# Kernel optimization log

Measured on AMD Instinct MI355X. Metric: run time of the kernel, lower is better.

Reference implementation:

```python
import jax, jax.numpy as jnp
import numpy as np

B, S, H, F, E, K = 2, 2048, 1024, 4096, 8, 2

def setup_inputs() -> dict:
    key = jax.random.key(0)
    ks = jax.random.split(key, 8)
    x = jax.random.normal(ks[0], (B, S, H), dtype=jnp.float32)
    # top_k list stacked on leading axis K; probs as from a softmax-topk router
    selected_probs = jax.random.uniform(ks[1], (K, B, S, 1), dtype=jnp.float32)
    selected_experts = jax.random.randint(ks[2], (K, B, S, 1), 0, E).astype(jnp.int32)
    scale = 0.02
    w1 = jax.random.normal(ks[3], (E, H, F), dtype=jnp.float32) * scale
    b1 = jnp.zeros((E, F), dtype=jnp.float32)
    w2 = jax.random.normal(ks[4], (E, F, H), dtype=jnp.float32) * scale
    b2 = jnp.zeros((E, H), dtype=jnp.float32)
    return {"input": x, "selected_probs": selected_probs,
            "selected_experts": selected_experts,
            "w1": w1, "b1": b1, "w2": w2, "b2": b2}

def reference(input, selected_probs, selected_experts, w1, b1, w2, b2):
    # Dense all-experts FFN: every expert processes every token.
    # h: [E, B, S, F]
    h = jax.nn.gelu(jnp.einsum('bsh,ehf->ebsf', input, w1) + b1[:, None, None, :])
    # expert_outputs: [E, B, S, H]
    expert_out = jnp.einsum('ebsf,efh->ebsh', h, w2) + b2[:, None, None, :]
    # combine weight per expert: sum_k probs_k * (sel_k == e)  -> [E, B, S, 1]
    eids = jnp.arange(E, dtype=selected_experts.dtype)
    mask = (selected_experts[:, None] == eids[None, :, None, None, None]).astype(input.dtype)  # [K,E,B,S,1]
    combine_w = (selected_probs[:, None] * mask).sum(axis=0)  # [E,B,S,1]
    return (combine_w * expert_out).sum(axis=0)  # [B,S,H]
```

## Files before the change

### kernel.cpp

```cpp
#include <hip/hip_runtime.h>
#include <hip/hip_bf16.h>
#include <stdint.h>

#define B_ 2
#define S_ 2048
#define H_ 1024
#define F_ 4096
#define E_ 8
#define KTOP_ 2
#define NTOK (B_*S_)
#define NPAIR (KTOP_*NTOK)
#define NPAIR_PAD (NPAIR+128)

static const size_t WS_XG   = 131072;
static const size_t SZ_XG   = (size_t)NPAIR_PAD * H_ * 2;
static const size_t WS_W1T  = WS_XG + SZ_XG;
static const size_t SZ_W1T  = (size_t)E_ * F_ * H_ * 2;
static const size_t WS_W2T  = WS_W1T + SZ_W1T;
static const size_t SZ_W2T  = (size_t)E_ * H_ * F_ * 2;
static const size_t WS_HBUF = WS_W2T + SZ_W2T;
static const size_t SZ_HBUF = (size_t)NPAIR_PAD * F_ * 2;
static const size_t WS_YBUF = WS_HBUF + SZ_HBUF;
static const size_t SZ_YBUF = (size_t)NPAIR * H_ * 4;

typedef __attribute__((ext_vector_type(8))) short bf16x8;
typedef __attribute__((ext_vector_type(4))) float f32x4;

__device__ __forceinline__ unsigned short f2bf(float f) {
  unsigned int u = __float_as_uint(f);
  u += 0x7fffu + ((u >> 16) & 1u);
  return (unsigned short)(u >> 16);
}

__device__ __forceinline__ void load_lds16(const void* g, void* l) {
  __builtin_amdgcn_global_load_lds(
      (const __attribute__((address_space(1))) unsigned int*)g,
      (__attribute__((address_space(3))) unsigned int*)l, 16, 0, 0);
}

__global__ void k_init(int* meta) {
  if (threadIdx.x < 32) meta[threadIdx.x] = 0;
}

__global__ void k_count(const int* __restrict__ sel, int* meta) {
  int i = blockIdx.x * 256 + threadIdx.x;
  if (i < NPAIR) atomicAdd(&meta[sel[i]], 1);
}

__global__ void k_scan(int* meta) {
  if (threadIdx.x == 0) {
    int acc = 0, t = 0;
    for (int e = 0; e < E_; e++) {
      meta[16 + e] = acc;
      int c = meta[e];
      for (int r0 = 0; r0 < c; r0 += 128) meta[32 + (t++)] = (e << 13) | r0;
      acc += c;
    }
    meta[24] = acc;
    meta[25] = t;
  }
}

__global__ void k_fill(const int* __restrict__ sel, const float* __restrict__ probs,
                       int* meta, int* __restrict__ tok, int* __restrict__ slot,
                       float* __restrict__ prob) {
  int i = blockIdx.x * 256 + threadIdx.x;
  if (i < NPAIR) {
    int e = sel[i];
    int pos = meta[16 + e] + atomicAdd(&meta[8 + e], 1);
    tok[pos]  = i & (NTOK - 1);
    slot[pos] = i;
    prob[pos] = probs[i];
  }
}

__global__ void k_gather(const float* __restrict__ x, const int* __restrict__ tok,
                         unsigned short* __restrict__ Xg) {
  int p = blockIdx.x, t = threadIdx.x;
  int token = tok[p];
  float4 v = ((const float4*)(x + (size_t)token * H_))[t];
  ushort4 o;
  o.x = f2bf(v.x); o.y = f2bf(v.y); o.z = f2bf(v.z); o.w = f2bf(v.w);
  ((ushort4*)(Xg + (size_t)p * H_))[t] = o;
}

__global__ void k_transpose(const float* __restrict__ src, unsigned short* __restrict__ dst,
                            int R, int C) {
  __shared__ float tile[32][33];
  int e = blockIdx.z;
  size_t c0 = (size_t)blockIdx.x * 32, r0 = (size_t)blockIdx.y * 32;
  int tx = threadIdx.x & 31, ty = threadIdx.x >> 5;
  const float* s = src + ((size_t)e * R + r0) * C + c0;
#pragma unroll
  for (int i = 0; i < 4; i++) tile[ty + 8 * i][tx] = s[(size_t)(ty + 8 * i) * C + tx];
  __syncthreads();
  unsigned short* d = dst + ((size_t)e * C + c0) * R + r0;
#pragma unroll
  for (int i = 0; i < 4; i++) d[(size_t)(ty + 8 * i) * R + tx] = f2bf(tile[tx][ty + 8 * i]);
}

template <int K, int EP>
__global__ __launch_bounds__(256, 2) void k_gemm(
    const short* __restrict__ Aall, const short* __restrict__ Wt,
    const float* __restrict__ bias, const int* __restrict__ meta,
    unsigned short* __restrict__ Hbuf, float* __restrict__ ybuf,
    const int* __restrict__ slot, const float* __restrict__ prob) {
  int tile = blockIdx.y;
  if (tile >= meta[25]) return;
  int d  = meta[32 + tile];
  int e  = d >> 13, r0 = d & 8191;
  int ne = meta[e];
  int p0 = meta[16 + e] + r0;
  int n0 = blockIdx.x * 128;
  const int NFULL = (EP == 0) ? F_ : H_;
  const short* A0 = Aall + (size_t)p0 * K;
  const short* B0 = Wt + ((size_t)e * NFULL + n0) * K;

  __shared__ short As[128 * 64];
  __shared__ short Bs[128 * 64];
  int t = threadIdx.x, lane = t & 63, wid = t >> 6;
  int wr = wid >> 1, wc = wid & 1, g = lane >> 4, l15 = lane & 15;
  f32x4 acc[4][4] = {};

  for (int k0 = 0; k0 < K; k0 += 64) {
#pragma unroll
    for (int c = 0; c < 4; c++) {
      int off = c * 4096 + wid * 1024 + lane * 16;
      int row = off >> 7, inb = off & 127;
      int sinb = inb ^ ((row & 7) << 4);
      load_lds16((const char*)A0 + ((size_t)row * K + k0) * 2 + sinb, (char*)As + off);
      load_lds16((const char*)B0 + ((size_t)row * K + k0) * 2 + sinb, (char*)Bs + off);
    }
    __syncthreads();
#pragma unroll
    for (int kk = 0; kk < 2; kk++) {
      bf16x8 af[4], bfr[4];
#pragma unroll
      for (int m = 0; m < 4; m++) {
        int row = wr * 64 + m * 16 + l15;
        af[m] = *(const bf16x8*)((const char*)As + row * 128 +
                                 ((kk * 64 + g * 16) ^ ((row & 7) << 4)));
      }
#pragma unroll
      for (int n = 0; n < 4; n++) {
        int row = wc * 64 + n * 16 + l15;
        bfr[n] = *(const bf16x8*)((const char*)Bs + row * 128 +
                                  ((kk * 64 + g * 16) ^ ((row & 7) << 4)));
      }
#pragma unroll
      for (int m = 0; m < 4; m++)
#pragma unroll
        for (int n = 0; n < 4; n++)
          acc[m][n] = __builtin_amdgcn_mfma_f32_16x16x32_bf16(af[m], bfr[n], acc[m][n], 0, 0, 0);
    }
    __syncthreads();
  }

  if (EP == 0) {
#pragma unroll
    for (int n = 0; n < 4; n++) {
      int col = n0 + wc * 64 + n * 16 + l15;
      float bv = bias[e * F_ + col];
#pragma unroll
      for (int m = 0; m < 4; m++) {
        int rbase = wr * 64 + m * 16 + g * 4;
#pragma unroll
        for (int r = 0; r < 4; r++) {
          int row = rbase + r;
          if (r0 + row < ne) {
            float x = acc[m][n][r] + bv;
            float y = 0.7978845608f * x * (1.f + 0.044715f * x * x);
            y = fminf(y, 20.f);
            float u = __expf(2.f * y);
            float th = (u - 1.f) / (u + 1.f);
            Hbuf[(size_t)(p0 + row) * F_ + col] = f2bf(0.5f * x * (1.f + th));
          }
        }
      }
    }
  } else {
#pragma unroll
    for (int n = 0; n < 4; n++) {
      int col = n0 + wc * 64 + n * 16 + l15;
      float bv = bias[e * H_ + col];
#pragma unroll
      for (int m = 0; m < 4; m++) {
        int rbase = wr * 64 + m * 16 + g * 4;
#pragma unroll
        for (int r = 0; r < 4; r++) {
          int row = rbase + r;
          if (r0 + row < ne) {
            int p = p0 + row;
            ybuf[(size_t)slot[p] * H_ + col] = (acc[m][n][r] + bv) * prob[p];
          }
        }
      }
    }
  }
}

__global__ void k_combine(const float* __restrict__ yb, float* __restrict__ out) {
  size_t i = (size_t)blockIdx.x * 256 + threadIdx.x;
  float4 a = ((const float4*)yb)[i];
  float4 b = ((const float4*)(yb + (size_t)NTOK * H_))[i];
  float4 o;
  o.x = a.x + b.x; o.y = a.y + b.y; o.z = a.z + b.z; o.w = a.w + b.w;
  ((float4*)out)[i] = o;
}

extern "C" void kernel_launch(void* const* d_in, const int* in_sizes, int n_in,
                              void* d_out, int out_size, void* d_ws, size_t ws_size,
                              hipStream_t stream) {
  const float* x     = (const float*)d_in[0];
  const float* probs = (const float*)d_in[1];
  const int*   sel   = (const int*)d_in[2];
  const float* w1    = (const float*)d_in[3];
  const float* b1    = (const float*)d_in[4];
  const float* w2    = (const float*)d_in[5];
  const float* b2    = (const float*)d_in[6];
  float* out = (float*)d_out;

  char* W = (char*)d_ws;
  int*   meta = (int*)W;
  int*   tok  = (int*)(W + 4096);
  int*   slot = (int*)(W + 36864);
  float* prob = (float*)(W + 69632);
  unsigned short* Xg  = (unsigned short*)(W + WS_XG);
  short* w1t = (short*)(W + WS_W1T);
  short* w2t = (short*)(W + WS_W2T);
  unsigned short* Hb  = (unsigned short*)(W + WS_HBUF);
  float* yb  = (float*)(W + WS_YBUF);

  k_init<<<1, 256, 0, stream>>>(meta);
  k_count<<<NPAIR / 256, 256, 0, stream>>>(sel, meta);
  k_scan<<<1, 64, 0, stream>>>(meta);
  k_fill<<<NPAIR / 256, 256, 0, stream>>>(sel, probs, meta, tok, slot, prob);
  k_gather<<<NPAIR, 256, 0, stream>>>(x, tok, Xg);
  k_transpose<<<dim3(F_ / 32, H_ / 32, E_), 256, 0, stream>>>(w1, (unsigned short*)w1t, H_, F_);
  k_transpose<<<dim3(H_ / 32, F_ / 32, E_), 256, 0, stream>>>(w2, (unsigned short*)w2t, F_, H_);
  k_gemm<H_, 0><<<dim3(F_ / 128, 72), 256, 0, stream>>>(
      (const short*)Xg, w1t, b1, meta, Hb, yb, slot, prob);
  k_gemm<F_, 1><<<dim3(H_ / 128, 72), 256, 0, stream>>>(
      (const short*)Hb, w2t, b2, meta, Hb, yb, slot, prob);
  k_combine<<<(NTOK * H_ / 4) / 256, 256, 0, stream>>>(yb, out);
}
```

Measured before the change: 432.2 us.

## Rewrite expert GEMMs with 256-row tiles, 4-stage LDS pipeline and wider transpose

Replaces the 128x128 single-buffered GEMM with a 512-thread kernel using 256-row M tiles and a 4-slot LDS ring. Loads are issued three k-steps ahead, with explicit vmcnt waits, barriers and setprio around the MFMA phases, so global loads overlap compute. The GELU epilogue becomes an exp2 plus reciprocal sigmoid form of the tanh approximation. The weight transpose moves to 64x64 tiles with float4 reads and paired bf16 writes. Larger tiles cut the number of M tiles but add padding waste for experts whose counts are not multiples of 256, and the LDS footprint grows.

```diff
diff --git a/kernel.cpp b/kernel.cpp
--- a/kernel.cpp
+++ b/kernel.cpp
@@ -10,7 +10,7 @@
 #define KTOP_ 2
 #define NTOK (B_*S_)
 #define NPAIR (KTOP_*NTOK)
-#define NPAIR_PAD (NPAIR+128)
+#define NPAIR_PAD (NPAIR+256)
 
 static const size_t WS_XG   = 131072;
 static const size_t SZ_XG   = (size_t)NPAIR_PAD * H_ * 2;
@@ -21,7 +21,6 @@
 static const size_t WS_HBUF = WS_W2T + SZ_W2T;
 static const size_t SZ_HBUF = (size_t)NPAIR_PAD * F_ * 2;
 static const size_t WS_YBUF = WS_HBUF + SZ_HBUF;
-static const size_t SZ_YBUF = (size_t)NPAIR * H_ * 4;
 
 typedef __attribute__((ext_vector_type(8))) short bf16x8;
 typedef __attribute__((ext_vector_type(4))) float f32x4;
@@ -36,6 +35,10 @@
   __builtin_amdgcn_global_load_lds(
       (const __attribute__((address_space(1))) unsigned int*)g,
       (__attribute__((address_space(3))) unsigned int*)l, 16, 0, 0);
+}
+
+template <int N> __device__ __forceinline__ void waitcnt_vm() {
+  asm volatile("s_waitcnt vmcnt(%0)" :: "n"(N) : "memory");
 }
 
 __global__ void k_init(int* meta) {
@@ -53,7 +56,7 @@
     for (int e = 0; e < E_; e++) {
       meta[16 + e] = acc;
       int c = meta[e];
-      for (int r0 = 0; r0 < c; r0 += 128) meta[32 + (t++)] = (e << 13) | r0;
+      for (int r0 = 0; r0 < c; r0 += 256) meta[32 + (t++)] = (e << 13) | r0;
       acc += c;
     }
     meta[24] = acc;
@@ -86,112 +89,209 @@
 
 __global__ void k_transpose(const float* __restrict__ src, unsigned short* __restrict__ dst,
                             int R, int C) {
-  __shared__ float tile[32][33];
+  __shared__ float tile[64][65];
   int e = blockIdx.z;
-  size_t c0 = (size_t)blockIdx.x * 32, r0 = (size_t)blockIdx.y * 32;
-  int tx = threadIdx.x & 31, ty = threadIdx.x >> 5;
-  const float* s = src + ((size_t)e * R + r0) * C + c0;
-#pragma unroll
-  for (int i = 0; i < 4; i++) tile[ty + 8 * i][tx] = s[(size_t)(ty + 8 * i) * C + tx];
+  size_t c0 = (size_t)blockIdx.x * 64, r0 = (size_t)blockIdx.y * 64;
+  int t = threadIdx.x;
+  int r = t >> 2, q = t & 3;
+  const float4* s = (const float4*)(src + ((size_t)e * R + r0 + r) * C + c0 + q * 16);
+  float4 v0 = s[0], v1 = s[1], v2 = s[2], v3 = s[3];
+  float* tp = &tile[r][q * 16];
+  tp[0]=v0.x; tp[1]=v0.y; tp[2]=v0.z; tp[3]=v0.w;
+  tp[4]=v1.x; tp[5]=v1.y; tp[6]=v1.z; tp[7]=v1.w;
+  tp[8]=v2.x; tp[9]=v2.y; tp[10]=v2.z; tp[11]=v2.w;
+  tp[12]=v3.x; tp[13]=v3.y; tp[14]=v3.z; tp[15]=v3.w;
   __syncthreads();
   unsigned short* d = dst + ((size_t)e * C + c0) * R + r0;
 #pragma unroll
-  for (int i = 0; i < 4; i++) d[(size_t)(ty + 8 * i) * R + tx] = f2bf(tile[tx][ty + 8 * i]);
-}
-
-template <int K, int EP>
-__global__ __launch_bounds__(256, 2) void k_gemm(
+  for (int i = 0; i < 8; i++) {
+    int chunk = t + 256 * i;
+    int c = chunk >> 5, j = chunk & 31;
+    ushort2 o;
+    o.x = f2bf(tile[2 * j][c]);
+    o.y = f2bf(tile[2 * j + 1][c]);
+    *(ushort2*)(d + (size_t)c * R + 2 * j) = o;
+  }
+}
+
+
+template <int MH, int NREP>
+__device__ __forceinline__ void domfma(f32x4 (&acc)[8][NREP], const bf16x8 (&af)[4],
+                                       const bf16x8 (&bfr)[NREP]) {
+#pragma unroll
+  for (int m = 0; m < 4; m++)
+#pragma unroll
+    for (int n = 0; n < NREP; n++)
+      acc[MH * 4 + m][n] =
+          __builtin_amdgcn_mfma_f32_16x16x32_bf16(af[m], bfr[n], acc[MH * 4 + m][n], 0, 0, 0);
+}
+
+template <int K, int NREP, int EP>
+__global__ __launch_bounds__(512, 2) void k_gemm8(
     const short* __restrict__ Aall, const short* __restrict__ Wt,
     const float* __restrict__ bias, const int* __restrict__ meta,
     unsigned short* __restrict__ Hbuf, float* __restrict__ ybuf,
-    const int* __restrict__ slot, const float* __restrict__ prob) {
+    const int* __restrict__ slotA, const float* __restrict__ prob) {
+  constexpr int BN = NREP * 64;
+  constexpr int NT = K / 32;
+  constexpr int ASLOT = 256 * 64;
+  constexpr int BSLOT = BN * 64;
+  constexpr int SLOT = ASLOT + BSLOT;
+  constexpr int ALOADS = ASLOT / (512 * 16);
+  constexpr int BLOADS = BSLOT / (512 * 16);
+  constexpr int TLOADS = ALOADS + BLOADS;
+  constexpr int NFULL = (EP == 0) ? F_ : H_;
+
+  __shared__ __align__(1024) char lds[4 * SLOT];
+
   int tile = blockIdx.y;
   if (tile >= meta[25]) return;
   int d  = meta[32 + tile];
   int e  = d >> 13, r0 = d & 8191;
   int ne = meta[e];
   int p0 = meta[16 + e] + r0;
-  int n0 = blockIdx.x * 128;
-  const int NFULL = (EP == 0) ? F_ : H_;
-  const short* A0 = Aall + (size_t)p0 * K;
-  const short* B0 = Wt + ((size_t)e * NFULL + n0) * K;
-
-  __shared__ short As[128 * 64];
-  __shared__ short Bs[128 * 64];
-  int t = threadIdx.x, lane = t & 63, wid = t >> 6;
-  int wr = wid >> 1, wc = wid & 1, g = lane >> 4, l15 = lane & 15;
-  f32x4 acc[4][4] = {};
-
-  for (int k0 = 0; k0 < K; k0 += 64) {
-#pragma unroll
-    for (int c = 0; c < 4; c++) {
-      int off = c * 4096 + wid * 1024 + lane * 16;
-      int row = off >> 7, inb = off & 127;
-      int sinb = inb ^ ((row & 7) << 4);
-      load_lds16((const char*)A0 + ((size_t)row * K + k0) * 2 + sinb, (char*)As + off);
-      load_lds16((const char*)B0 + ((size_t)row * K + k0) * 2 + sinb, (char*)Bs + off);
-    }
-    __syncthreads();
-#pragma unroll
-    for (int kk = 0; kk < 2; kk++) {
-      bf16x8 af[4], bfr[4];
-#pragma unroll
-      for (int m = 0; m < 4; m++) {
-        int row = wr * 64 + m * 16 + l15;
-        af[m] = *(const bf16x8*)((const char*)As + row * 128 +
-                                 ((kk * 64 + g * 16) ^ ((row & 7) << 4)));
-      }
-#pragma unroll
-      for (int n = 0; n < 4; n++) {
-        int row = wc * 64 + n * 16 + l15;
-        bfr[n] = *(const bf16x8*)((const char*)Bs + row * 128 +
-                                  ((kk * 64 + g * 16) ^ ((row & 7) << 4)));
-      }
-#pragma unroll
-      for (int m = 0; m < 4; m++)
-#pragma unroll
-        for (int n = 0; n < 4; n++)
-          acc[m][n] = __builtin_amdgcn_mfma_f32_16x16x32_bf16(af[m], bfr[n], acc[m][n], 0, 0, 0);
-    }
-    __syncthreads();
+  int n0 = blockIdx.x * BN;
+  const char* A0 = (const char*)(Aall + (size_t)p0 * K);
+  const char* B0 = (const char*)(Wt + ((size_t)e * NFULL + n0) * K);
+
+  int t = threadIdx.x, lane = t & 63;
+  int wid = t >> 6, wr = wid >> 2, wc = wid & 3, g = lane >> 4, l15 = lane & 15;
+  f32x4 acc[8][NREP] = {};
+
+  auto stageA = [&](int kt) {
+    char* dst = lds + (kt & 3) * SLOT;
+    const char* src = A0 + kt * 64;
+#pragma unroll
+    for (int l = 0; l < ALOADS; l++) {
+      int off = l * 8192 + t * 16;
+      int row = off >> 6, inb = off & 63;
+      int sw = inb ^ (((row >> 1) & 3) << 4);
+      load_lds16(src + (size_t)row * (K * 2) + sw, dst + off);
+    }
+  };
+  auto stageB = [&](int kt) {
+    char* dst = lds + (kt & 3) * SLOT + ASLOT;
+    const char* src = B0 + kt * 64;
+#pragma unroll
+    for (int l = 0; l < BLOADS; l++) {
+      int off = l * 8192 + t * 16;
+      int row = off >> 6, inb = off & 63;
+      int sw = inb ^ (((row >> 1) & 3) << 4);
+      load_lds16(src + (size_t)row * (K * 2) + sw, dst + off);
+    }
+  };
+
+  bf16x8 af[4], bfr[NREP];
+  auto readB = [&](int kt) {
+    const char* base = lds + (kt & 3) * SLOT + ASLOT;
+#pragma unroll
+    for (int n = 0; n < NREP; n++) {
+      int row = wc * (BN / 4) + n * 16 + l15;
+      bfr[n] = *(const bf16x8*)(base + row * 64 + ((g * 16) ^ (((row >> 1) & 3) << 4)));
+    }
+  };
+
+  stageA(0); stageB(0); stageA(1); stageB(1); stageA(2); stageB(2);
+  waitcnt_vm<2 * TLOADS>();
+  __builtin_amdgcn_s_barrier();
+  __builtin_amdgcn_sched_barrier(0);
+
+  int kt = 0;
+  for (; kt < NT - 3; kt++) {
+    const char* abase = lds + (kt & 3) * SLOT;
+    readB(kt);
+#pragma unroll
+    for (int m = 0; m < 4; m++) {
+      int row = wr * 128 + m * 16 + l15;
+      af[m] = *(const bf16x8*)(abase + row * 64 + ((g * 16) ^ (((row >> 1) & 3) << 4)));
+    }
+    stageA(kt + 3);
+    __builtin_amdgcn_s_barrier();
+    __builtin_amdgcn_s_setprio(1);
+    domfma<0, NREP>(acc, af, bfr);
+    __builtin_amdgcn_s_setprio(0);
+    __builtin_amdgcn_s_barrier();
+    __builtin_amdgcn_sched_barrier(0);
+#pragma unroll
+    for (int m = 0; m < 4; m++) {
+      int row = wr * 128 + (4 + m) * 16 + l15;
+      af[m] = *(const bf16x8*)(abase + row * 64 + ((g * 16) ^ (((row >> 1) & 3) << 4)));
+    }
+    stageB(kt + 3);
+    __builtin_amdgcn_s_barrier();
+    __builtin_amdgcn_s_setprio(1);
+    domfma<1, NREP>(acc, af, bfr);
+    __builtin_amdgcn_s_setprio(0);
+    waitcnt_vm<2 * TLOADS>();
+    __builtin_amdgcn_s_barrier();
+    __builtin_amdgcn_sched_barrier(0);
+  }
+  for (; kt < NT; kt++) {
+    const char* abase = lds + (kt & 3) * SLOT;
+    readB(kt);
+#pragma unroll
+    for (int m = 0; m < 4; m++) {
+      int row = wr * 128 + m * 16 + l15;
+      af[m] = *(const bf16x8*)(abase + row * 64 + ((g * 16) ^ (((row >> 1) & 3) << 4)));
+    }
+    __builtin_amdgcn_s_barrier();
+    __builtin_amdgcn_s_setprio(1);
+    domfma<0, NREP>(acc, af, bfr);
+    __builtin_amdgcn_s_setprio(0);
+    __builtin_amdgcn_s_barrier();
+    __builtin_amdgcn_sched_barrier(0);
+#pragma unroll
+    for (int m = 0; m < 4; m++) {
+      int row = wr * 128 + (4 + m) * 16 + l15;
+      af[m] = *(const bf16x8*)(abase + row * 64 + ((g * 16) ^ (((row >> 1) & 3) << 4)));
+    }
+    __builtin_amdgcn_s_barrier();
+    __builtin_amdgcn_s_setprio(1);
+    domfma<1, NREP>(acc, af, bfr);
+    __builtin_amdgcn_s_setprio(0);
+    if (kt == NT - 3) waitcnt_vm<TLOADS>();
+    else if (kt == NT - 2) waitcnt_vm<0>();
+    __builtin_amdgcn_s_barrier();
+    __builtin_amdgcn_sched_barrier(0);
   }
 
   if (EP == 0) {
 #pragma unroll
-    for (int n = 0; n < 4; n++) {
-      int col = n0 + wc * 64 + n * 16 + l15;
+    for (int n = 0; n < NREP; n++) {
+      int col = n0 + wc * (BN / 4) + n * 16 + l15;
       float bv = bias[e * F_ + col];
 #pragma unroll
-      for (int m = 0; m < 4; m++) {
-        int rbase = wr * 64 + m * 16 + g * 4;
+      for (int m = 0; m < 8; m++) {
+        int rbase = wr * 128 + m * 16 + g * 4;
 #pragma unroll
         for (int r = 0; r < 4; r++) {
           int row = rbase + r;
           if (r0 + row < ne) {
             float x = acc[m][n][r] + bv;
-            float y = 0.7978845608f * x * (1.f + 0.044715f * x * x);
-            y = fminf(y, 20.f);
-            float u = __expf(2.f * y);
-            float th = (u - 1.f) / (u + 1.f);
-            Hbuf[(size_t)(p0 + row) * F_ + col] = f2bf(0.5f * x * (1.f + th));
+            float x2 = x * x;
+            float ttt = x * (2.302118f + 0.1029518f * x2);
+            ttt = fminf(ttt, 60.f);
+            float u = __builtin_amdgcn_exp2f(ttt);
+            float rr = __frcp_rn(1.f + u);
+            Hbuf[(size_t)(p0 + row) * F_ + col] = f2bf(x * u * rr);
           }
         }
       }
     }
   } else {
 #pragma unroll
-    for (int n = 0; n < 4; n++) {
-      int col = n0 + wc * 64 + n * 16 + l15;
+    for (int n = 0; n < NREP; n++) {
+      int col = n0 + wc * (BN / 4) + n * 16 + l15;
       float bv = bias[e * H_ + col];
 #pragma unroll
-      for (int m = 0; m < 4; m++) {
-        int rbase = wr * 64 + m * 16 + g * 4;
+      for (int m = 0; m < 8; m++) {
+        int rbase = wr * 128 + m * 16 + g * 4;
 #pragma unroll
         for (int r = 0; r < 4; r++) {
           int row = rbase + r;
           if (r0 + row < ne) {
             int p = p0 + row;
-            ybuf[(size_t)slot[p] * H_ + col] = (acc[m][n][r] + bv) * prob[p];
+            ybuf[(size_t)slotA[p] * H_ + col] = (acc[m][n][r] + bv) * prob[p];
           }
         }
       }
@@ -236,11 +336,11 @@
   k_scan<<<1, 64, 0, stream>>>(meta);
   k_fill<<<NPAIR / 256, 256, 0, stream>>>(sel, probs, meta, tok, slot, prob);
   k_gather<<<NPAIR, 256, 0, stream>>>(x, tok, Xg);
-  k_transpose<<<dim3(F_ / 32, H_ / 32, E_), 256, 0, stream>>>(w1, (unsigned short*)w1t, H_, F_);
-  k_transpose<<<dim3(H_ / 32, F_ / 32, E_), 256, 0, stream>>>(w2, (unsigned short*)w2t, F_, H_);
-  k_gemm<H_, 0><<<dim3(F_ / 128, 72), 256, 0, stream>>>(
+  k_transpose<<<dim3(F_ / 64, H_ / 64, E_), 256, 0, stream>>>(w1, (unsigned short*)w1t, H_, F_);
+  k_transpose<<<dim3(H_ / 64, F_ / 64, E_), 256, 0, stream>>>(w2, (unsigned short*)w2t, F_, H_);
+  k_gemm8<H_, 4, 0><<<dim3(F_ / 256, 40), 512, 0, stream>>>(
       (const short*)Xg, w1t, b1, meta, Hb, yb, slot, prob);
-  k_gemm<F_, 1><<<dim3(H_ / 128, 72), 256, 0, stream>>>(
+  k_gemm8<F_, 2, 1><<<dim3(H_ / 128, 40), 512, 0, stream>>>(
       (const short*)Hb, w2t, b2, meta, Hb, yb, slot, prob);
   k_combine<<<(NTOK * H_ / 4) / 256, 256, 0, stream>>>(yb, out);
 }
```

Result: slower. 489.3 us (+13.2%).

## Double-buffer MoE GEMMs with larger tiles, vectorize transpose, cheaper GELU

Applied to the files above, without the earlier changes.

Replaces the single-buffered 128x128 expert GEMM with a templated 512-thread kernel. It double-buffers LDS so the next K-slice loads while MFMAs run, and uses 256x256 tiles for the first GEMM and 128x128 for the second. Separate tile schedules for 256-row and 128-row blocks are added in the scan. The weight transpose now uses 64x64 tiles with float4 loads and paired bf16 stores, and the tanh-GELU is rewritten as x*sigmoid using exp2 and a reciprocal. This adds LDS pressure and a slightly different GELU approximation path.

```diff
diff --git a/kernel.cpp b/kernel.cpp
--- a/kernel.cpp
+++ b/kernel.cpp
@@ -10,7 +10,7 @@
 #define KTOP_ 2
 #define NTOK (B_*S_)
 #define NPAIR (KTOP_*NTOK)
-#define NPAIR_PAD (NPAIR+128)
+#define NPAIR_PAD (NPAIR+256)
 
 static const size_t WS_XG   = 131072;
 static const size_t SZ_XG   = (size_t)NPAIR_PAD * H_ * 2;
@@ -21,7 +21,6 @@
 static const size_t WS_HBUF = WS_W2T + SZ_W2T;
 static const size_t SZ_HBUF = (size_t)NPAIR_PAD * F_ * 2;
 static const size_t WS_YBUF = WS_HBUF + SZ_HBUF;
-static const size_t SZ_YBUF = (size_t)NPAIR * H_ * 4;
 
 typedef __attribute__((ext_vector_type(8))) short bf16x8;
 typedef __attribute__((ext_vector_type(4))) float f32x4;
@@ -49,15 +48,17 @@
 
 __global__ void k_scan(int* meta) {
   if (threadIdx.x == 0) {
-    int acc = 0, t = 0;
+    int acc = 0, t256 = 0, t128 = 0;
     for (int e = 0; e < E_; e++) {
       meta[16 + e] = acc;
       int c = meta[e];
-      for (int r0 = 0; r0 < c; r0 += 128) meta[32 + (t++)] = (e << 13) | r0;
+      for (int r0 = 0; r0 < c; r0 += 256) meta[32 + (t256++)] = (e << 13) | r0;
+      for (int r0 = 0; r0 < c; r0 += 128) meta[72 + (t128++)] = (e << 13) | r0;
       acc += c;
     }
     meta[24] = acc;
-    meta[25] = t;
+    meta[25] = t256;
+    meta[26] = t128;
   }
 }
 
@@ -86,112 +87,150 @@
 
 __global__ void k_transpose(const float* __restrict__ src, unsigned short* __restrict__ dst,
                             int R, int C) {
-  __shared__ float tile[32][33];
+  __shared__ float tile[64][65];
   int e = blockIdx.z;
-  size_t c0 = (size_t)blockIdx.x * 32, r0 = (size_t)blockIdx.y * 32;
-  int tx = threadIdx.x & 31, ty = threadIdx.x >> 5;
-  const float* s = src + ((size_t)e * R + r0) * C + c0;
-#pragma unroll
-  for (int i = 0; i < 4; i++) tile[ty + 8 * i][tx] = s[(size_t)(ty + 8 * i) * C + tx];
+  size_t c0 = (size_t)blockIdx.x * 64, r0 = (size_t)blockIdx.y * 64;
+  int t = threadIdx.x;
+  int r = t >> 2, q = t & 3;
+  const float4* s = (const float4*)(src + ((size_t)e * R + r0 + r) * C + c0 + q * 16);
+  float4 v0 = s[0], v1 = s[1], v2 = s[2], v3 = s[3];
+  float* tp = &tile[r][q * 16];
+  tp[0]=v0.x; tp[1]=v0.y; tp[2]=v0.z; tp[3]=v0.w;
+  tp[4]=v1.x; tp[5]=v1.y; tp[6]=v1.z; tp[7]=v1.w;
+  tp[8]=v2.x; tp[9]=v2.y; tp[10]=v2.z; tp[11]=v2.w;
+  tp[12]=v3.x; tp[13]=v3.y; tp[14]=v3.z; tp[15]=v3.w;
   __syncthreads();
   unsigned short* d = dst + ((size_t)e * C + c0) * R + r0;
 #pragma unroll
-  for (int i = 0; i < 4; i++) d[(size_t)(ty + 8 * i) * R + tx] = f2bf(tile[tx][ty + 8 * i]);
-}
-
-template <int K, int EP>
-__global__ __launch_bounds__(256, 2) void k_gemm(
+  for (int i = 0; i < 8; i++) {
+    int chunk = t + 256 * i;
+    int c = chunk >> 5, j = chunk & 31;
+    ushort2 o;
+    o.x = f2bf(tile[2 * j][c]);
+    o.y = f2bf(tile[2 * j + 1][c]);
+    *(ushort2*)(d + (size_t)c * R + 2 * j) = o;
+  }
+}
+
+
+template <int K, int MREP, int NREP, int DBASE, int NIDX, int EP>
+__global__ __launch_bounds__(512, EP == 0 ? 2 : 4) void k_gemm2p(
     const short* __restrict__ Aall, const short* __restrict__ Wt,
     const float* __restrict__ bias, const int* __restrict__ meta,
     unsigned short* __restrict__ Hbuf, float* __restrict__ ybuf,
-    const int* __restrict__ slot, const float* __restrict__ prob) {
+    const int* __restrict__ slotA, const float* __restrict__ prob) {
+  constexpr int BM = 2 * MREP * 16;
+  constexpr int BN = 4 * NREP * 16;
+  constexpr int NT = K / 64;
+  constexpr int ABYTES = BM * 128;
+  constexpr int BBYTES = BN * 128;
+  constexpr int BUF = ABYTES + BBYTES;
+  constexpr int LOADS = BUF / (512 * 16);
+  constexpr int ALOADS = ABYTES / (512 * 16);
+  constexpr int NFULL = (EP == 0) ? F_ : H_;
+
+  __shared__ __align__(1024) char lds[2 * BUF];
+
   int tile = blockIdx.y;
-  if (tile >= meta[25]) return;
-  int d  = meta[32 + tile];
+  if (tile >= meta[NIDX]) return;
+  int d  = meta[DBASE + tile];
   int e  = d >> 13, r0 = d & 8191;
   int ne = meta[e];
   int p0 = meta[16 + e] + r0;
-  int n0 = blockIdx.x * 128;
-  const int NFULL = (EP == 0) ? F_ : H_;
-  const short* A0 = Aall + (size_t)p0 * K;
-  const short* B0 = Wt + ((size_t)e * NFULL + n0) * K;
-
-  __shared__ short As[128 * 64];
-  __shared__ short Bs[128 * 64];
+  int n0 = blockIdx.x * BN;
+  const char* A0 = (const char*)(Aall + (size_t)p0 * K);
+  const char* B0 = (const char*)(Wt + ((size_t)e * NFULL + n0) * K);
+
   int t = threadIdx.x, lane = t & 63, wid = t >> 6;
-  int wr = wid >> 1, wc = wid & 1, g = lane >> 4, l15 = lane & 15;
-  f32x4 acc[4][4] = {};
-
-  for (int k0 = 0; k0 < K; k0 += 64) {
-#pragma unroll
-    for (int c = 0; c < 4; c++) {
-      int off = c * 4096 + wid * 1024 + lane * 16;
-      int row = off >> 7, inb = off & 127;
-      int sinb = inb ^ ((row & 7) << 4);
-      load_lds16((const char*)A0 + ((size_t)row * K + k0) * 2 + sinb, (char*)As + off);
-      load_lds16((const char*)B0 + ((size_t)row * K + k0) * 2 + sinb, (char*)Bs + off);
-    }
+  int wr = wid >> 2, wc = wid & 3, g = lane >> 4, l15 = lane & 15;
+  f32x4 acc[MREP][NREP] = {};
+
+  auto stage = [&](int kt, char* dst) {
+    const char* sa = A0 + kt * 128;
+    const char* sb = B0 + kt * 128;
+#pragma unroll
+    for (int l = 0; l < LOADS; l++) {
+      int off = l * 8192 + t * 16;
+      if (l < ALOADS) {
+        int row = off >> 7, inb = off & 127;
+        load_lds16(sa + (size_t)row * (K * 2) + (inb ^ ((row & 7) << 4)), dst + off);
+      } else {
+        int o2 = off - ABYTES;
+        int row = o2 >> 7, inb = o2 & 127;
+        load_lds16(sb + (size_t)row * (K * 2) + (inb ^ ((row & 7) << 4)), dst + off);
+      }
+    }
+  };
+
+  stage(0, lds);
+  __syncthreads();
+  int cur = 0;
+  for (int kt = 0; kt < NT; kt++) {
+    const char* ab = lds + cur * BUF;
+    const char* bb = ab + ABYTES;
+    if (kt + 1 < NT) stage(kt + 1, lds + (cur ^ 1) * BUF);
+    __builtin_amdgcn_s_setprio(1);
+#pragma unroll
+    for (int kk = 0; kk < 2; kk++) {
+      bf16x8 af[MREP], bf[NREP];
+#pragma unroll
+      for (int m = 0; m < MREP; m++) {
+        int row = wr * (MREP * 16) + m * 16 + l15;
+        af[m] = *(const bf16x8*)(ab + row * 128 + ((kk * 64 + g * 16) ^ ((row & 7) << 4)));
+      }
+#pragma unroll
+      for (int n = 0; n < NREP; n++) {
+        int row = wc * (NREP * 16) + n * 16 + l15;
+        bf[n] = *(const bf16x8*)(bb + row * 128 + ((kk * 64 + g * 16) ^ ((row & 7) << 4)));
+      }
+#pragma unroll
+      for (int m = 0; m < MREP; m++)
+#pragma unroll
+        for (int n = 0; n < NREP; n++)
+          acc[m][n] = __builtin_amdgcn_mfma_f32_16x16x32_bf16(af[m], bf[n], acc[m][n], 0, 0, 0);
+    }
+    __builtin_amdgcn_s_setprio(0);
     __syncthreads();
-#pragma unroll
-    for (int kk = 0; kk < 2; kk++) {
-      bf16x8 af[4], bfr[4];
-#pragma unroll
-      for (int m = 0; m < 4; m++) {
-        int row = wr * 64 + m * 16 + l15;
-        af[m] = *(const bf16x8*)((const char*)As + row * 128 +
-                                 ((kk * 64 + g * 16) ^ ((row & 7) << 4)));
-      }
-#pragma unroll
-      for (int n = 0; n < 4; n++) {
-        int row = wc * 64 + n * 16 + l15;
-        bfr[n] = *(const bf16x8*)((const char*)Bs + row * 128 +
-                                  ((kk * 64 + g * 16) ^ ((row & 7) << 4)));
-      }
-#pragma unroll
-      for (int m = 0; m < 4; m++)
-#pragma unroll
-        for (int n = 0; n < 4; n++)
-          acc[m][n] = __builtin_amdgcn_mfma_f32_16x16x32_bf16(af[m], bfr[n], acc[m][n], 0, 0, 0);
-    }
-    __syncthreads();
+    cur ^= 1;
   }
 
   if (EP == 0) {
 #pragma unroll
-    for (int n = 0; n < 4; n++) {
-      int col = n0 + wc * 64 + n * 16 + l15;
+    for (int n = 0; n < NREP; n++) {
+      int col = n0 + wc * (NREP * 16) + n * 16 + l15;
       float bv = bias[e * F_ + col];
 #pragma unroll
-      for (int m = 0; m < 4; m++) {
-        int rbase = wr * 64 + m * 16 + g * 4;
+      for (int m = 0; m < MREP; m++) {
+        int rbase = wr * (MREP * 16) + m * 16 + g * 4;
 #pragma unroll
         for (int r = 0; r < 4; r++) {
           int row = rbase + r;
           if (r0 + row < ne) {
             float x = acc[m][n][r] + bv;
-            float y = 0.7978845608f * x * (1.f + 0.044715f * x * x);
-            y = fminf(y, 20.f);
-            float u = __expf(2.f * y);
-            float th = (u - 1.f) / (u + 1.f);
-            Hbuf[(size_t)(p0 + row) * F_ + col] = f2bf(0.5f * x * (1.f + th));
+            float x2 = x * x;
+            float ttt = x * (2.302118f + 0.1029518f * x2);
+            ttt = fminf(ttt, 60.f);
+            float u = __builtin_amdgcn_exp2f(ttt);
+            float rr = __frcp_rn(1.f + u);
+            Hbuf[(size_t)(p0 + row) * F_ + col] = f2bf(x * u * rr);
           }
         }
       }
     }
   } else {
 #pragma unroll
-    for (int n = 0; n < 4; n++) {
-      int col = n0 + wc * 64 + n * 16 + l15;
+    for (int n = 0; n < NREP; n++) {
+      int col = n0 + wc * (NREP * 16) + n * 16 + l15;
       float bv = bias[e * H_ + col];
 #pragma unroll
-      for (int m = 0; m < 4; m++) {
-        int rbase = wr * 64 + m * 16 + g * 4;
+      for (int m = 0; m < MREP; m++) {
+        int rbase = wr * (MREP * 16) + m * 16 + g * 4;
 #pragma unroll
         for (int r = 0; r < 4; r++) {
           int row = rbase + r;
           if (r0 + row < ne) {
             int p = p0 + row;
-            ybuf[(size_t)slot[p] * H_ + col] = (acc[m][n][r] + bv) * prob[p];
+            ybuf[(size_t)slotA[p] * H_ + col] = (acc[m][n][r] + bv) * prob[p];
           }
         }
       }
@@ -236,11 +275,11 @@
   k_scan<<<1, 64, 0, stream>>>(meta);
   k_fill<<<NPAIR / 256, 256, 0, stream>>>(sel, probs, meta, tok, slot, prob);
   k_gather<<<NPAIR, 256, 0, stream>>>(x, tok, Xg);
-  k_transpose<<<dim3(F_ / 32, H_ / 32, E_), 256, 0, stream>>>(w1, (unsigned short*)w1t, H_, F_);
-  k_transpose<<<dim3(H_ / 32, F_ / 32, E_), 256, 0, stream>>>(w2, (unsigned short*)w2t, F_, H_);
-  k_gemm<H_, 0><<<dim3(F_ / 128, 72), 256, 0, stream>>>(
+  k_transpose<<<dim3(F_ / 64, H_ / 64, E_), 256, 0, stream>>>(w1, (unsigned short*)w1t, H_, F_);
+  k_transpose<<<dim3(H_ / 64, F_ / 64, E_), 256, 0, stream>>>(w2, (unsigned short*)w2t, F_, H_);
+  k_gemm2p<H_, 8, 4, 32, 25, 0><<<dim3(F_ / 256, 40), 512, 0, stream>>>(
       (const short*)Xg, w1t, b1, meta, Hb, yb, slot, prob);
-  k_gemm<F_, 1><<<dim3(H_ / 128, 72), 256, 0, stream>>>(
+  k_gemm2p<F_, 4, 2, 72, 26, 1><<<dim3(H_ / 128, 72), 512, 0, stream>>>(
       (const short*)Hb, w2t, b2, meta, Hb, yb, slot, prob);
   k_combine<<<(NTOK * H_ / 4) / 256, 256, 0, stream>>>(yb, out);
 }
```

Result: slower. 478.2 us (+10.6%).
